# Optimization experiments

Hardware: AMD Instinct MI355X
Metric: run time of the kernel (lower is better)

The kernel has to match this reference:

```python
import jax, jax.numpy as jnp
import numpy as np

N, E, D, ED, H, DH = 30000, 480000, 128, 64, 8, 16  # nodes, edges, node dim, edge dim, heads, dim/head


def _bn(x, g, b):
    # BatchNorm1d training-mode math: biased batch stats over the node/edge axis
    m = jnp.mean(x, axis=0)
    v = jnp.mean(jnp.square(x - m), axis=0)
    return g * (x - m) * jax.lax.rsqrt(v + 1e-5) + b


def setup_inputs() -> dict:
    key = jax.random.key(0)
    ks = jax.random.split(key, 32)
    w = lambda k, shp: (jax.random.normal(k, shp, dtype=jnp.float32) * 0.05)
    inp = {
        "x": jax.random.normal(ks[0], (N, D), dtype=jnp.float32),
        "edge_index": jax.random.randint(ks[1], (2, E), 0, N, dtype=jnp.int32),
        "edge_attr": jax.random.normal(ks[2], (E, ED), dtype=jnp.float32),
        # attention projections (use_bias=False)
        "Wq": w(ks[3], (D, D)), "Wk": w(ks[4], (D, D)), "Wv": w(ks[5], (D, D)),
        "We": w(ks[6], (ED, D)),
        # output / edge projections
        "W_Oh": w(ks[7], (D, D)), "b_Oh": jnp.zeros((D,), jnp.float32),
        "W_ep": w(ks[8], (H, ED)), "b_ep": jnp.zeros((ED,), jnp.float32),
        "W_Oe": w(ks[9], (ED, ED)), "b_Oe": jnp.zeros((ED,), jnp.float32),
        # FFNs
        "W_h1": w(ks[10], (D, 2 * D)), "b_h1": jnp.zeros((2 * D,), jnp.float32),
        "W_h2": w(ks[11], (2 * D, D)), "b_h2": jnp.zeros((D,), jnp.float32),
        "W_e1": w(ks[12], (ED, 2 * ED)), "b_e1": jnp.zeros((2 * ED,), jnp.float32),
        "W_e2": w(ks[13], (2 * ED, ED)), "b_e2": jnp.zeros((ED,), jnp.float32),
        # batch-norm affine params
        "g1h": jnp.ones((D,), jnp.float32), "B1h": jnp.zeros((D,), jnp.float32),
        "g1e": jnp.ones((ED,), jnp.float32), "B1e": jnp.zeros((ED,), jnp.float32),
        "g2h": jnp.ones((D,), jnp.float32), "B2h": jnp.zeros((D,), jnp.float32),
        "g2e": jnp.ones((ED,), jnp.float32), "B2e": jnp.zeros((ED,), jnp.float32),
    }
    return inp


def reference(x, edge_index, edge_attr, Wq, Wk, Wv, We,
              W_Oh, b_Oh, W_ep, b_ep, W_Oe, b_Oe,
              W_h1, b_h1, W_h2, b_h2, W_e1, b_e1, W_e2, b_e2,
              g1h, B1h, g1e, B1e, g2h, B2h, g2e, B2e):
    n = x.shape[0]
    e_n = edge_attr.shape[0]
    src, dst = edge_index[0], edge_index[1]

    # MultiHeadAttentionLayer
    Q = (x @ Wq).reshape(n, H, DH)
    K = (x @ Wk).reshape(n, H, DH)
    V = (x @ Wv).reshape(n, H, DH)
    Pe = (edge_attr @ We).reshape(e_n, H, DH)

    inv_sqrt_d = 1.0 / np.sqrt(DH).astype(np.float32)
    score = jnp.sum(Q[dst] * K[src] * inv_sqrt_d * Pe, axis=-1)  # [E, H]
    e_out = score
    sc = jnp.exp(jnp.clip(score, -5.0, 5.0))
    z = jax.ops.segment_sum(sc, dst, num_segments=n)            # [N, H]
    alpha = sc / (z[dst] + 1e-6)                                # [E, H]
    msg = V[src] * alpha[..., None]                             # [E, H, DH]
    h_attn = jax.ops.segment_sum(msg, dst, num_segments=n).reshape(n, H * DH)

    # edge_project on raw scores, then O projections (dropout=0)
    e = e_out @ W_ep + b_ep
    h = h_attn @ W_Oh + b_Oh
    e = e @ W_Oe + b_Oe

    # residual 1 (in_dim == out_dim, edge dims equal -> identity residuals)
    h = x + h
    e = edge_attr + e

    h = _bn(h, g1h, B1h)
    e = _bn(e, g1e, B1e)

    # FFNs with residual + BN
    h2 = h
    h = jax.nn.relu(h @ W_h1 + b_h1) @ W_h2 + b_h2
    h = _bn(h2 + h, g2h, B2h)

    e2 = e
    e = jax.nn.relu(e @ W_e1 + b_e1) @ W_e2 + b_e2
    e = _bn(e2 + e, g2e, B2e)

    return (h, e)
```

## Files before the change

kernel.cpp:

```cpp
#include <hip/hip_runtime.h>
#include <hip/hip_bf16.h>

typedef __hip_bfloat16 bf16;

#define NN 30000
#define NE 480000
#define DD 128
#define ED 64
#define NH 8

#define ST_SUM_H1 0
#define ST_SQ_H1  128
#define ST_SUM_H2 256
#define ST_SQ_H2  384
#define ST_SUM_E1 512
#define ST_SQ_E1  576
#define ST_SUM_E2 640
#define ST_SQ_E2  704
#define W_FLAG    768

#define W_HATT  241024
#define W_SC    4081024

#define CSR_DEG   12000000
#define CSR_ROW   12030000
#define CSR_CUR   12060004
#define CSR_ADJ   12100000

__device__ __forceinline__ float ldf(const void* p, long i, bool bf) {
  if (bf) return __bfloat162float(((const bf16*)p)[i]);
  return ((const float*)p)[i];
}

__global__ __launch_bounds__(64) void k_detect(const void* __restrict__ x, int* __restrict__ flag)
{
  int lane = threadIdx.x;
  unsigned w = ((const unsigned*)x)[lane];
  unsigned low = w & 0xFFFFu;
  unsigned el = (low >> 7) & 0xFFu;
  bool hit = (el >= 0x70u && el <= 0x86u);
  unsigned long long m = __ballot(hit);
  if (lane == 0) *flag = (__popcll(m) >= 32) ? 1 : 0;
}

__global__ __launch_bounds__(256) void k_deg(const int* __restrict__ ei, int* __restrict__ deg)
{
  int i = blockIdx.x * 256 + threadIdx.x;
  if (i < NE) atomicAdd(&deg[ei[NE + i]], 1);
}

__global__ __launch_bounds__(1024) void k_scan(
    const int* __restrict__ deg, int* __restrict__ rowptr, int* __restrict__ cursor)
{
  __shared__ int buf[1024];
  __shared__ int carry;
  int tid = threadIdx.x;
  if (tid == 0) carry = 0;
  __syncthreads();
  for (int c = 0; c < 30; ++c) {
    int i = c * 1024 + tid;
    int v = (i < NN) ? deg[i] : 0;
    buf[tid] = v;
    __syncthreads();
    for (int off = 1; off < 1024; off <<= 1) {
      int t = (tid >= off) ? buf[tid - off] : 0;
      __syncthreads();
      buf[tid] += t;
      __syncthreads();
    }
    int excl = carry + buf[tid] - v;
    if (i < NN) { rowptr[i] = excl; cursor[i] = excl; }
    if (i == NN) rowptr[NN] = excl;
    __syncthreads();
    if (tid == 1023) carry += buf[1023];
    __syncthreads();
  }
}

__global__ __launch_bounds__(256) void k_fill(
    const int* __restrict__ ei, int* __restrict__ cursor, int* __restrict__ adj)
{
  int i = blockIdx.x * 256 + threadIdx.x;
  if (i < NE) {
    int p = atomicAdd(&cursor[ei[NE + i]], 1);
    adj[p] = i;
  }
}

__global__ __launch_bounds__(128) void k_qkv(
    const void* __restrict__ x, const void* __restrict__ Wq,
    const void* __restrict__ Wk, const void* __restrict__ Wv,
    float* __restrict__ Q, float* __restrict__ Kb, float* __restrict__ V,
    const int* __restrict__ flag)
{
  const bool isbf = (*flag != 0);
  __shared__ float xs[128][36];
  int tid = threadIdx.x;
  int row0 = blockIdx.x * 32;
  int nrows = min(32, NN - row0);
  for (int r = 0; r < 32; ++r)
    xs[tid][r] = (r < nrows) ? ldf(x, (long)(row0 + r) * DD + tid, isbf) : 0.f;
  __syncthreads();
  int c0 = (tid & 63) * 2;
  int rh = (tid >> 6) * 16;
  const void* Ws[3] = {Wq, Wk, Wv};
  float* Os[3] = {Q, Kb, V};
  for (int mm = 0; mm < 3; ++mm) {
    const void* W = Ws[mm];
    float u0[16], u1[16];
    #pragma unroll
    for (int r = 0; r < 16; ++r) { u0[r] = 0.f; u1[r] = 0.f; }
    #pragma unroll 4
    for (int k = 0; k < 128; ++k) {
      float w0 = ldf(W, (long)k * DD + c0, isbf);
      float w1 = ldf(W, (long)k * DD + c0 + 1, isbf);
      const float4* xp = (const float4*)&xs[k][rh];
      #pragma unroll
      for (int r4 = 0; r4 < 4; ++r4) {
        float4 x4 = xp[r4];
        u0[r4*4+0] += x4.x * w0; u1[r4*4+0] += x4.x * w1;
        u0[r4*4+1] += x4.y * w0; u1[r4*4+1] += x4.y * w1;
        u0[r4*4+2] += x4.z * w0; u1[r4*4+2] += x4.z * w1;
        u0[r4*4+3] += x4.w * w0; u1[r4*4+3] += x4.w * w1;
      }
    }
    float* O = Os[mm];
    #pragma unroll
    for (int r = 0; r < 16; ++r) {
      if (rh + r < nrows)
        *(float2*)&O[(long)(row0 + rh + r) * DD + c0] = make_float2(u0[r], u1[r]);
    }
  }
}

__global__ __launch_bounds__(128) void k_edge_score(
    const int* __restrict__ ei, const void* __restrict__ ea,
    const void* __restrict__ We, const float* __restrict__ Q,
    const float* __restrict__ Kb,
    float* __restrict__ score, const int* __restrict__ flag)
{
  const bool isbf = (*flag != 0);
  __shared__ float es[64][36];
  __shared__ int sd_s[32], sd_d[32];
  int tid = threadIdx.x;
  long e0 = (long)blockIdx.x * 32;
  #pragma unroll
  for (int i = 0; i < 16; ++i) {
    int idx = i * 128 + tid;
    es[idx & 63][idx >> 6] = ldf(ea, e0 * ED + idx, isbf);
  }
  if (tid < 32) sd_s[tid] = ei[e0 + tid];
  else if (tid < 64) sd_d[tid - 32] = ei[NE + e0 + (tid - 32)];
  __syncthreads();
  float pe[32];
  #pragma unroll
  for (int r = 0; r < 32; ++r) pe[r] = 0.f;
  #pragma unroll 4
  for (int k = 0; k < 64; ++k) {
    float w = ldf(We, (long)k * DD + tid, isbf);
    const float4* ep = (const float4*)&es[k][0];
    #pragma unroll
    for (int r4 = 0; r4 < 8; ++r4) {
      float4 e4 = ep[r4];
      pe[r4*4+0] += e4.x * w; pe[r4*4+1] += e4.y * w;
      pe[r4*4+2] += e4.z * w; pe[r4*4+3] += e4.w * w;
    }
  }
  int h = tid >> 4;
  bool lead = (tid & 15) == 0;
  #pragma unroll 4
  for (int r = 0; r < 32; ++r) {
    int s = sd_s[r], d = sd_d[r];
    float q  = Q [(long)d * DD + tid];
    float kk = Kb[(long)s * DD + tid];
    float sv = q * kk * pe[r];
    sv += __shfl_xor(sv, 1);
    sv += __shfl_xor(sv, 2);
    sv += __shfl_xor(sv, 4);
    sv += __shfl_xor(sv, 8);
    if (lead) score[(e0 + r) * NH + h] = sv * 0.25f;
  }
}

__global__ __launch_bounds__(256) void k_aggregate(
    const int* __restrict__ ei, const float* __restrict__ V,
    const float* __restrict__ score, const int* __restrict__ rowptr,
    const int* __restrict__ adj, float* __restrict__ hatt)
{
  int lane = threadIdx.x & 63;
  int wv = threadIdx.x >> 6;
  int d = blockIdx.x * 4 + wv;
  if (d >= NN) return;
  int p0 = rowptr[d], p1 = rowptr[d + 1];
  int hsh = lane >> 3;
  float a0 = 0.f, a1 = 0.f, zh = 0.f;
  for (int p = p0; p < p1; ++p) {
    int e = adj[p];
    int s = ei[e];
    float sc = score[(long)e * NH + hsh];
    float ec = __expf(fminf(fmaxf(sc, -5.f), 5.f));
    float2 v = *(const float2*)(V + (long)s * DD + 2 * lane);
    a0 += ec * v.x; a1 += ec * v.y; zh += ec;
  }
  float inv = 1.f / (zh + 1e-6f);
  *(float2*)(hatt + (long)d * DD + 2 * lane) = make_float2(a0 * inv, a1 * inv);
}

__global__ __launch_bounds__(128) void k_edge_proj(
    const void* __restrict__ ea, const float* __restrict__ score,
    const void* __restrict__ W_ep, const void* __restrict__ b_ep,
    const void* __restrict__ W_Oe, const void* __restrict__ b_Oe,
    float* __restrict__ eout, float* __restrict__ stats,
    const int* __restrict__ flag)
{
  const bool isbf = (*flag != 0);
  __shared__ float sc[32][9];
  __shared__ float ep_lds[64][36];
  __shared__ float rs[2][64], rq[2][64];
  int tid = threadIdx.x;
  int j = tid & 63, wv = tid >> 6, rh = wv * 16;
  float bep = ldf(b_ep, j, isbf), boe = ldf(b_Oe, j, isbf);
  float wep[8];
  #pragma unroll
  for (int hh = 0; hh < 8; ++hh) wep[hh] = ldf(W_ep, hh * ED + j, isbf);
  float lsum = 0.f, lsq = 0.f;
  for (int t = blockIdx.x; t < NE / 32; t += gridDim.x) {
    long e0 = (long)t * 32;
    __syncthreads();
    #pragma unroll
    for (int i = 0; i < 2; ++i) {
      int idx = i * 128 + tid;
      sc[idx >> 3][idx & 7] = score[e0 * NH + idx];
    }
    __syncthreads();
    float u[16];
    #pragma unroll
    for (int r = 0; r < 16; ++r) u[r] = bep;
    #pragma unroll
    for (int hh = 0; hh < 8; ++hh) {
      float w = wep[hh];
      #pragma unroll
      for (int r = 0; r < 16; ++r) u[r] += sc[rh + r][hh] * w;
    }
    #pragma unroll
    for (int r = 0; r < 16; ++r) ep_lds[j][rh + r] = u[r];
    __syncthreads();
    float acc[16];
    #pragma unroll
    for (int r = 0; r < 16; ++r) acc[r] = 0.f;
    #pragma unroll 4
    for (int k = 0; k < 64; ++k) {
      float w = ldf(W_Oe, (long)k * ED + j, isbf);
      const float4* up = (const float4*)&ep_lds[k][rh];
      #pragma unroll
      for (int r4 = 0; r4 < 4; ++r4) {
        float4 u4 = up[r4];
        acc[r4*4+0] += u4.x * w; acc[r4*4+1] += u4.y * w;
        acc[r4*4+2] += u4.z * w; acc[r4*4+3] += u4.w * w;
      }
    }
    #pragma unroll
    for (int r = 0; r < 16; ++r) {
      float v = ldf(ea, (e0 + rh + r) * ED + j, isbf) + acc[r] + boe;
      eout[(e0 + rh + r) * ED + j] = v;
      lsum += v; lsq += v * v;
    }
  }
  rs[wv][j] = lsum; rq[wv][j] = lsq;
  __syncthreads();
  if (wv == 0) {
    atomicAdd(&stats[ST_SUM_E1 + j], rs[0][j] + rs[1][j]);
    atomicAdd(&stats[ST_SQ_E1 + j], rq[0][j] + rq[1][j]);
  }
}

__global__ __launch_bounds__(128) void k_hproj(
    const float* __restrict__ hatt, const void* __restrict__ x,
    const void* __restrict__ W_Oh, const void* __restrict__ b_Oh,
    float* __restrict__ hout, float* __restrict__ stats,
    const int* __restrict__ flag)
{
  const bool isbf = (*flag != 0);
  __shared__ float hs[128][36];
  __shared__ float ssum[2][128], ssq[2][128];
  int tid = threadIdx.x;
  int row0 = blockIdx.x * 32;
  int nrows = min(32, NN - row0);
  for (int r = 0; r < 32; ++r)
    hs[tid][r] = (r < nrows) ? hatt[(long)(row0 + r) * DD + tid] : 0.f;
  __syncthreads();
  int c0 = (tid & 63) * 2;
  int wv = tid >> 6;
  int rh = wv * 16;
  float u0[16], u1[16];
  #pragma unroll
  for (int r = 0; r < 16; ++r) { u0[r] = 0.f; u1[r] = 0.f; }
  #pragma unroll 4
  for (int k = 0; k < 128; ++k) {
    float w0 = ldf(W_Oh, (long)k * DD + c0, isbf);
    float w1 = ldf(W_Oh, (long)k * DD + c0 + 1, isbf);
    const float4* hp = (const float4*)&hs[k][rh];
    #pragma unroll
    for (int r4 = 0; r4 < 4; ++r4) {
      float4 h4 = hp[r4];
      u0[r4*4+0] += h4.x * w0; u1[r4*4+0] += h4.x * w1;
      u0[r4*4+1] += h4.y * w0; u1[r4*4+1] += h4.y * w1;
      u0[r4*4+2] += h4.z * w0; u1[r4*4+2] += h4.z * w1;
      u0[r4*4+3] += h4.w * w0; u1[r4*4+3] += h4.w * w1;
    }
  }
  float bo0 = ldf(b_Oh, c0, isbf), bo1 = ldf(b_Oh, c0 + 1, isbf);
  float s0 = 0.f, q0 = 0.f, s1 = 0.f, q1 = 0.f;
  #pragma unroll
  for (int r = 0; r < 16; ++r) {
    if (rh + r < nrows) {
      long row = row0 + rh + r;
      float v0 = ldf(x, row * DD + c0, isbf) + u0[r] + bo0;
      float v1 = ldf(x, row * DD + c0 + 1, isbf) + u1[r] + bo1;
      *(float2*)&hout[row * DD + c0] = make_float2(v0, v1);
      s0 += v0; q0 += v0 * v0; s1 += v1; q1 += v1 * v1;
    }
  }
  ssum[wv][c0] = s0; ssum[wv][c0 + 1] = s1;
  ssq[wv][c0] = q0;  ssq[wv][c0 + 1] = q1;
  __syncthreads();
  atomicAdd(&stats[ST_SUM_H1 + tid], ssum[0][tid] + ssum[1][tid]);
  atomicAdd(&stats[ST_SQ_H1 + tid], ssq[0][tid] + ssq[1][tid]);
}

__global__ __launch_bounds__(128) void k_hffn(
    float* __restrict__ hio,
    const void* __restrict__ g1h, const void* __restrict__ B1h,
    const void* __restrict__ W_h1, const void* __restrict__ b_h1,
    const void* __restrict__ W_h2, const void* __restrict__ b_h2,
    float* __restrict__ stats, const int* __restrict__ flag)
{
  const bool isbf = (*flag != 0);
  __shared__ float hb[128][36];
  __shared__ float uu[256][36];
  __shared__ float ssum[2][128], ssq[2][128];
  int tid = threadIdx.x;
  int row0 = blockIdx.x * 32;
  int nrows = min(32, NN - row0);
  float m = stats[ST_SUM_H1 + tid] * (1.0f / NN);
  float var = stats[ST_SQ_H1 + tid] * (1.0f / NN) - m * m;
  float rstd = rsqrtf(fmaxf(var, 0.f) + 1e-5f);
  float g = ldf(g1h, tid, isbf), B = ldf(B1h, tid, isbf);
  for (int r = 0; r < 32; ++r) {
    float v = (r < nrows) ? hio[(long)(row0 + r) * DD + tid] : 0.f;
    hb[tid][r] = g * (v - m) * rstd + B;
  }
  __syncthreads();
  float u0[32], u1[32];
  #pragma unroll
  for (int r = 0; r < 32; ++r) { u0[r] = 0.f; u1[r] = 0.f; }
  #pragma unroll 2
  for (int k = 0; k < 128; ++k) {
    float w0 = ldf(W_h1, (long)k * 256 + tid, isbf);
    float w1 = ldf(W_h1, (long)k * 256 + 128 + tid, isbf);
    const float4* hp = (const float4*)&hb[k][0];
    #pragma unroll
    for (int r4 = 0; r4 < 8; ++r4) {
      float4 h4 = hp[r4];
      u0[r4*4+0] += h4.x * w0; u1[r4*4+0] += h4.x * w1;
      u0[r4*4+1] += h4.y * w0; u1[r4*4+1] += h4.y * w1;
      u0[r4*4+2] += h4.z * w0; u1[r4*4+2] += h4.z * w1;
      u0[r4*4+3] += h4.w * w0; u1[r4*4+3] += h4.w * w1;
    }
  }
  float bu0 = ldf(b_h1, tid, isbf), bu1 = ldf(b_h1, 128 + tid, isbf);
  for (int r = 0; r < 32; ++r) {
    uu[tid][r]       = fmaxf(u0[r] + bu0, 0.f);
    uu[128 + tid][r] = fmaxf(u1[r] + bu1, 0.f);
  }
  __syncthreads();
  int c0 = (tid & 63) * 2;
  int wv2 = tid >> 6;
  int rh2 = wv2 * 16;
  float f0[16], f1[16];
  #pragma unroll
  for (int r = 0; r < 16; ++r) { f0[r] = 0.f; f1[r] = 0.f; }
  #pragma unroll 2
  for (int jj = 0; jj < 256; ++jj) {
    float w0 = ldf(W_h2, (long)jj * DD + c0, isbf);
    float w1 = ldf(W_h2, (long)jj * DD + c0 + 1, isbf);
    const float4* up = (const float4*)&uu[jj][rh2];
    #pragma unroll
    for (int r4 = 0; r4 < 4; ++r4) {
      float4 u4 = up[r4];
      f0[r4*4+0] += u4.x * w0; f1[r4*4+0] += u4.x * w1;
      f0[r4*4+1] += u4.y * w0; f1[r4*4+1] += u4.y * w1;
      f0[r4*4+2] += u4.z * w0; f1[r4*4+2] += u4.z * w1;
      f0[r4*4+3] += u4.w * w0; f1[r4*4+3] += u4.w * w1;
    }
  }
  float bf0 = ldf(b_h2, c0, isbf), bf1 = ldf(b_h2, c0 + 1, isbf);
  float s0 = 0.f, q0 = 0.f, s1 = 0.f, q1 = 0.f;
  #pragma unroll
  for (int r = 0; r < 16; ++r) {
    if (rh2 + r < nrows) {
      float t0 = hb[c0][rh2 + r] + f0[r] + bf0;
      float t1 = hb[c0 + 1][rh2 + r] + f1[r] + bf1;
      *(float2*)&hio[(long)(row0 + rh2 + r) * DD + c0] = make_float2(t0, t1);
      s0 += t0; q0 += t0 * t0; s1 += t1; q1 += t1 * t1;
    }
  }
  ssum[wv2][c0] = s0; ssum[wv2][c0 + 1] = s1;
  ssq[wv2][c0] = q0;  ssq[wv2][c0 + 1] = q1;
  __syncthreads();
  atomicAdd(&stats[ST_SUM_H2 + tid], ssum[0][tid] + ssum[1][tid]);
  atomicAdd(&stats[ST_SQ_H2 + tid], ssq[0][tid] + ssq[1][tid]);
}

__global__ __launch_bounds__(256) void k_hfinal(
    float* __restrict__ io, const void* __restrict__ g,
    const void* __restrict__ B, const float* __restrict__ stats,
    const int* __restrict__ flag)
{
  const bool isbf = (*flag != 0);
  long idx = ((long)blockIdx.x * 256 + threadIdx.x) * 4;
  int c = (int)(idx & (DD - 1));
  float4 v = *(float4*)(io + idx);
  float o[4] = {v.x, v.y, v.z, v.w};
  #pragma unroll
  for (int j = 0; j < 4; ++j) {
    int cc = c + j;
    float m = stats[ST_SUM_H2 + cc] * (1.0f / NN);
    float var = stats[ST_SQ_H2 + cc] * (1.0f / NN) - m * m;
    float rstd = rsqrtf(fmaxf(var, 0.f) + 1e-5f);
    o[j] = ldf(g, cc, isbf) * (o[j] - m) * rstd + ldf(B, cc, isbf);
  }
  *(float4*)(io + idx) = make_float4(o[0], o[1], o[2], o[3]);
}

__global__ __launch_bounds__(128) void k_effn(
    float* __restrict__ eio,
    const void* __restrict__ g1e, const void* __restrict__ B1e,
    const void* __restrict__ W_e1, const void* __restrict__ b_e1,
    const void* __restrict__ W_e2, const void* __restrict__ b_e2,
    float* __restrict__ stats, const int* __restrict__ flag)
{
  const bool isbf = (*flag != 0);
  __shared__ float es[64][36];
  __shared__ float uu[128][36];
  __shared__ float rs[2][64], rq[2][64];
  int tid = threadIdx.x;
  int f = tid & 63;
  int wv = tid >> 6;
  int rh = wv * 16;
  long row0 = (long)blockIdx.x * 32;
  float m = stats[ST_SUM_E1 + f] * (1.0f / NE);
  float var = stats[ST_SQ_E1 + f] * (1.0f / NE) - m * m;
  float rstd = rsqrtf(fmaxf(var, 0.f) + 1e-5f);
  float g = ldf(g1e, f, isbf), B = ldf(B1e, f, isbf);
  #pragma unroll
  for (int r = 0; r < 16; ++r) {
    float v = eio[(row0 + rh + r) * ED + f];
    es[f][rh + r] = g * (v - m) * rstd + B;
  }
  __syncthreads();
  float u[32];
  #pragma unroll
  for (int r = 0; r < 32; ++r) u[r] = 0.f;
  #pragma unroll 4
  for (int k = 0; k < 64; ++k) {
    float w = ldf(W_e1, (long)k * 128 + tid, isbf);
    const float4* ep = (const float4*)&es[k][0];
    #pragma unroll
    for (int r4 = 0; r4 < 8; ++r4) {
      float4 e4 = ep[r4];
      u[r4*4+0] += e4.x * w; u[r4*4+1] += e4.y * w;
      u[r4*4+2] += e4.z * w; u[r4*4+3] += e4.w * w;
    }
  }
  float bu = ldf(b_e1, tid, isbf);
  #pragma unroll
  for (int r = 0; r < 32; ++r) uu[tid][r] = fmaxf(u[r] + bu, 0.f);
  __syncthreads();
  float acc[16];
  #pragma unroll
  for (int r = 0; r < 16; ++r) acc[r] = 0.f;
  #pragma unroll 4
  for (int j = 0; j < 128; ++j) {
    float w = ldf(W_e2, (long)j * ED + f, isbf);
    const float4* up = (const float4*)&uu[j][rh];
    #pragma unroll
    for (int r4 = 0; r4 < 4; ++r4) {
      float4 u4 = up[r4];
      acc[r4*4+0] += u4.x * w; acc[r4*4+1] += u4.y * w;
      acc[r4*4+2] += u4.z * w; acc[r4*4+3] += u4.w * w;
    }
  }
  float bf2 = ldf(b_e2, f, isbf);
  float lsum = 0.f, lsq = 0.f;
  #pragma unroll
  for (int r = 0; r < 16; ++r) {
    float t = es[f][rh + r] + acc[r] + bf2;
    eio[(row0 + rh + r) * ED + f] = t;
    lsum += t; lsq += t * t;
  }
  rs[wv][f] = lsum; rq[wv][f] = lsq;
  __syncthreads();
  if (wv == 0) {
    atomicAdd(&stats[ST_SUM_E2 + f], rs[0][f] + rs[1][f]);
    atomicAdd(&stats[ST_SQ_E2 + f], rq[0][f] + rq[1][f]);
  }
}

__global__ __launch_bounds__(256) void k_efinal(
    float* __restrict__ io, const void* __restrict__ g,
    const void* __restrict__ B, const float* __restrict__ stats,
    const int* __restrict__ flag)
{
  const bool isbf = (*flag != 0);
  long idx = ((long)blockIdx.x * 256 + threadIdx.x) * 4;
  int c = (int)(idx & (ED - 1));
  float4 v = *(float4*)(io + idx);
  float o[4] = {v.x, v.y, v.z, v.w};
  #pragma unroll
  for (int j = 0; j < 4; ++j) {
    int cc = c + j;
    float m = stats[ST_SUM_E2 + cc] * (1.0f / NE);
    float var = stats[ST_SQ_E2 + cc] * (1.0f / NE) - m * m;
    float rstd = rsqrtf(fmaxf(var, 0.f) + 1e-5f);
    o[j] = ldf(g, cc, isbf) * (o[j] - m) * rstd + ldf(B, cc, isbf);
  }
  *(float4*)(io + idx) = make_float4(o[0], o[1], o[2], o[3]);
}

extern "C" void kernel_launch(void* const* d_in, const int* in_sizes, int n_in,
                              void* d_out, int out_size, void* d_ws, size_t ws_size,
                              hipStream_t stream) {
  const void* x    = d_in[0];
  const int*  ei   = (const int*)d_in[1];
  const void* ea   = d_in[2];
  const void* Wq   = d_in[3];
  const void* Wk   = d_in[4];
  const void* Wv   = d_in[5];
  const void* We   = d_in[6];
  const void* W_Oh = d_in[7];
  const void* b_Oh = d_in[8];
  const void* W_ep = d_in[9];
  const void* b_ep = d_in[10];
  const void* W_Oe = d_in[11];
  const void* b_Oe = d_in[12];
  const void* W_h1 = d_in[13];
  const void* b_h1 = d_in[14];
  const void* W_h2 = d_in[15];
  const void* b_h2 = d_in[16];
  const void* W_e1 = d_in[17];
  const void* b_e1 = d_in[18];
  const void* W_e2 = d_in[19];
  const void* b_e2 = d_in[20];
  const void* g1h  = d_in[21];
  const void* B1h  = d_in[22];
  const void* g1e  = d_in[23];
  const void* B1e  = d_in[24];
  const void* g2h  = d_in[25];
  const void* B2h  = d_in[26];
  const void* g2e  = d_in[27];
  const void* B2e  = d_in[28];

  float* ws    = (float*)d_ws;
  float* stats = ws;
  int*   flag  = (int*)(ws + W_FLAG);
  float* hatt  = ws + W_HATT;
  float* score = ws + W_SC;

  float* out  = (float*)d_out;
  float* hout = out;
  float* eout = out + (size_t)NN * DD;
  float* Q    = out;
  float* Kb   = out + 3840000;
  float* V    = out + 7680000;
  int* deg    = (int*)out + CSR_DEG;
  int* rowptr = (int*)out + CSR_ROW;
  int* cursor = (int*)out + CSR_CUR;
  int* adj    = (int*)out + CSR_ADJ;

  hipMemsetAsync(ws, 0, 1024 * sizeof(float), stream);
  hipMemsetAsync(deg, 0, NN * sizeof(int), stream);
  k_detect<<<1, 64, 0, stream>>>(x, flag);

  k_deg <<<1875, 256, 0, stream>>>(ei, deg);
  k_scan<<<1, 1024, 0, stream>>>(deg, rowptr, cursor);
  k_fill<<<1875, 256, 0, stream>>>(ei, cursor, adj);

  k_qkv<<<938, 128, 0, stream>>>(x, Wq, Wk, Wv, Q, Kb, V, flag);
  k_edge_score<<<15000, 128, 0, stream>>>(ei, ea, We, Q, Kb, score, flag);
  k_aggregate<<<7500, 256, 0, stream>>>(ei, V, score, rowptr, adj, hatt);
  k_edge_proj<<<2048, 128, 0, stream>>>(ea, score, W_ep, b_ep, W_Oe, b_Oe, eout, stats, flag);
  k_hproj<<<938, 128, 0, stream>>>(hatt, x, W_Oh, b_Oh, hout, stats, flag);
  k_hffn<<<938, 128, 0, stream>>>(hout, g1h, B1h, W_h1, b_h1, W_h2, b_h2, stats, flag);
  k_hfinal<<<3750, 256, 0, stream>>>(hout, g2h, B2h, stats, flag);
  k_effn<<<15000, 128, 0, stream>>>(eout, g1e, B1e, W_e1, b_e1, W_e2, b_e2, stats, flag);
  k_efinal<<<30000, 256, 0, stream>>>(eout, g2e, B2e, stats, flag);
}
```

Measured before the change: 1.830 ms.

## Run edge FFN on bf16 MFMA with pre-transposed swizzled weights in LDS

The edge FFN (64->128->64 over 480k edges) moves from scalar fp32 FMAs to bf16 MFMA 16x16x32 instructions. Weights are transposed and converted to bf16 once by a new prep kernel, then staged per block in XOR-swizzled LDS along with the BN-normalised edge tile. The intent is to cut the compute-bound FMA cost of this large kernel. In exchange, the intermediate and the residual are rounded to bf16, which adds precision loss when the inputs are fp32.

```diff
diff --git a/kernel.cpp b/kernel.cpp
--- a/kernel.cpp
+++ b/kernel.cpp
@@ -2,6 +2,8 @@
 #include <hip/hip_bf16.h>
 
 typedef __hip_bfloat16 bf16;
+typedef __attribute__((ext_vector_type(8))) short short8v;
+typedef __attribute__((ext_vector_type(4))) float f32x4;
 
 #define NN 30000
 #define NE 480000
@@ -19,6 +21,8 @@
 #define ST_SQ_E2  704
 #define W_FLAG    768
 
+#define W_W1T   1024
+#define W_W2T   5120
 #define W_HATT  241024
 #define W_SC    4081024
 
@@ -30,6 +34,15 @@
 __device__ __forceinline__ float ldf(const void* p, long i, bool bf) {
   if (bf) return __bfloat162float(((const bf16*)p)[i]);
   return ((const float*)p)[i];
+}
+
+__device__ __forceinline__ unsigned short f2b(float f) {
+  unsigned u = __float_as_uint(f);
+  unsigned r = (u + 0x7FFFu + ((u >> 16) & 1u)) >> 16;
+  return (unsigned short)r;
+}
+__device__ __forceinline__ float b2f(unsigned short b) {
+  return __uint_as_float(((unsigned)b) << 16);
 }
 
 __global__ __launch_bounds__(64) void k_detect(const void* __restrict__ x, int* __restrict__ flag)
@@ -41,6 +54,23 @@
   bool hit = (el >= 0x70u && el <= 0x86u);
   unsigned long long m = __ballot(hit);
   if (lane == 0) *flag = (__popcll(m) >= 32) ? 1 : 0;
+}
+
+__global__ __launch_bounds__(256) void k_wprep(
+    const void* __restrict__ W_e1, const void* __restrict__ W_e2,
+    unsigned short* __restrict__ w1t, unsigned short* __restrict__ w2t,
+    const int* __restrict__ flag)
+{
+  const bool isbf = (*flag != 0);
+  int i = blockIdx.x * 256 + threadIdx.x;
+  if (i < 8192) {
+    int k = i >> 7, n = i & 127;
+    w1t[n * 64 + k] = f2b(ldf(W_e1, i, isbf));
+  } else {
+    int j = i - 8192;
+    int k = j >> 6, n = j & 63;
+    w2t[n * 128 + k] = f2b(ldf(W_e2, j, isbf));
+  }
 }
 
 __global__ __launch_bounds__(256) void k_deg(const int* __restrict__ ei, int* __restrict__ deg)
@@ -433,77 +463,134 @@
   *(float4*)(io + idx) = make_float4(o[0], o[1], o[2], o[3]);
 }
 
-__global__ __launch_bounds__(128) void k_effn(
+__global__ __launch_bounds__(256) void k_effn(
     float* __restrict__ eio,
     const void* __restrict__ g1e, const void* __restrict__ B1e,
-    const void* __restrict__ W_e1, const void* __restrict__ b_e1,
-    const void* __restrict__ W_e2, const void* __restrict__ b_e2,
+    const unsigned short* __restrict__ w1t, const unsigned short* __restrict__ w2t,
+    const void* __restrict__ b_e1, const void* __restrict__ b_e2,
     float* __restrict__ stats, const int* __restrict__ flag)
 {
   const bool isbf = (*flag != 0);
-  __shared__ float es[64][36];
-  __shared__ float uu[128][36];
-  __shared__ float rs[2][64], rq[2][64];
+  __shared__ unsigned short es[64 * 64];
+  __shared__ unsigned short uu[64 * 128];
+  __shared__ unsigned short w1[128 * 64];
+  __shared__ unsigned short w2[64 * 128];
+  __shared__ float ssum[4][64], ssq[4][64];
   int tid = threadIdx.x;
-  int f = tid & 63;
-  int wv = tid >> 6;
-  int rh = wv * 16;
-  long row0 = (long)blockIdx.x * 32;
-  float m = stats[ST_SUM_E1 + f] * (1.0f / NE);
-  float var = stats[ST_SQ_E1 + f] * (1.0f / NE) - m * m;
-  float rstd = rsqrtf(fmaxf(var, 0.f) + 1e-5f);
-  float g = ldf(g1e, f, isbf), B = ldf(B1e, f, isbf);
-  #pragma unroll
-  for (int r = 0; r < 16; ++r) {
-    float v = eio[(row0 + rh + r) * ED + f];
-    es[f][rh + r] = g * (v - m) * rstd + B;
-  }
-  __syncthreads();
-  float u[32];
-  #pragma unroll
-  for (int r = 0; r < 32; ++r) u[r] = 0.f;
-  #pragma unroll 4
-  for (int k = 0; k < 64; ++k) {
-    float w = ldf(W_e1, (long)k * 128 + tid, isbf);
-    const float4* ep = (const float4*)&es[k][0];
-    #pragma unroll
-    for (int r4 = 0; r4 < 8; ++r4) {
-      float4 e4 = ep[r4];
-      u[r4*4+0] += e4.x * w; u[r4*4+1] += e4.y * w;
-      u[r4*4+2] += e4.z * w; u[r4*4+3] += e4.w * w;
-    }
-  }
-  float bu = ldf(b_e1, tid, isbf);
-  #pragma unroll
-  for (int r = 0; r < 32; ++r) uu[tid][r] = fmaxf(u[r] + bu, 0.f);
-  __syncthreads();
-  float acc[16];
-  #pragma unroll
-  for (int r = 0; r < 16; ++r) acc[r] = 0.f;
-  #pragma unroll 4
-  for (int j = 0; j < 128; ++j) {
-    float w = ldf(W_e2, (long)j * ED + f, isbf);
-    const float4* up = (const float4*)&uu[j][rh];
-    #pragma unroll
-    for (int r4 = 0; r4 < 4; ++r4) {
-      float4 u4 = up[r4];
-      acc[r4*4+0] += u4.x * w; acc[r4*4+1] += u4.y * w;
-      acc[r4*4+2] += u4.z * w; acc[r4*4+3] += u4.w * w;
-    }
-  }
-  float bf2 = ldf(b_e2, f, isbf);
-  float lsum = 0.f, lsq = 0.f;
-  #pragma unroll
-  for (int r = 0; r < 16; ++r) {
-    float t = es[f][rh + r] + acc[r] + bf2;
-    eio[(row0 + rh + r) * ED + f] = t;
-    lsum += t; lsq += t * t;
-  }
-  rs[wv][f] = lsum; rq[wv][f] = lsq;
-  __syncthreads();
-  if (wv == 0) {
-    atomicAdd(&stats[ST_SUM_E2 + f], rs[0][f] + rs[1][f]);
-    atomicAdd(&stats[ST_SQ_E2 + f], rq[0][f] + rq[1][f]);
+  int lane = tid & 63, w = tid >> 6;
+  int ml = lane & 15, kg = lane >> 4;
+  long e0 = (long)blockIdx.x * 64;
+  {
+    unsigned* du = (unsigned*)w1;
+    int k2 = (tid & 31) * 2;
+    #pragma unroll
+    for (int it = 0; it < 16; ++it) {
+      int widx = it * 256 + tid;
+      int n = widx >> 5;
+      unsigned v = ((const unsigned*)w1t)[widx];
+      du[(n * 64 + (k2 ^ ((n & 7) << 3))) >> 1] = v;
+    }
+  }
+  {
+    unsigned* du = (unsigned*)w2;
+    int k2 = (tid & 63) * 2;
+    #pragma unroll
+    for (int it = 0; it < 16; ++it) {
+      int widx = it * 256 + tid;
+      int n = widx >> 6;
+      unsigned v = ((const unsigned*)w2t)[widx];
+      du[(n * 128 + (k2 ^ ((n & 7) << 3))) >> 1] = v;
+    }
+  }
+  {
+    unsigned* du = (unsigned*)es;
+    int c2 = (tid & 31) * 2;
+    float m0 = stats[ST_SUM_E1 + c2] * (1.0f / NE);
+    float v0 = stats[ST_SQ_E1 + c2] * (1.0f / NE) - m0 * m0;
+    float r0 = rsqrtf(fmaxf(v0, 0.f) + 1e-5f);
+    float g0 = ldf(g1e, c2, isbf), B0 = ldf(B1e, c2, isbf);
+    float m1 = stats[ST_SUM_E1 + c2 + 1] * (1.0f / NE);
+    float v1 = stats[ST_SQ_E1 + c2 + 1] * (1.0f / NE) - m1 * m1;
+    float r1 = rsqrtf(fmaxf(v1, 0.f) + 1e-5f);
+    float g1 = ldf(g1e, c2 + 1, isbf), B1 = ldf(B1e, c2 + 1, isbf);
+    #pragma unroll
+    for (int it = 0; it < 8; ++it) {
+      int widx = it * 256 + tid;
+      int r = widx >> 5;
+      float2 v = *(const float2*)(eio + (e0 + r) * 64 + c2);
+      unsigned short b0 = f2b(g0 * (v.x - m0) * r0 + B0);
+      unsigned short b1 = f2b(g1 * (v.y - m1) * r1 + B1);
+      du[(r * 64 + (c2 ^ ((r & 7) << 3))) >> 1] = (unsigned)b0 | ((unsigned)b1 << 16);
+    }
+  }
+  __syncthreads();
+  short8v a1[2];
+  #pragma unroll
+  for (int kt = 0; kt < 2; ++kt) {
+    int row = w * 16 + ml;
+    a1[kt] = *(short8v*)&es[row * 64 + ((kt * 32 + kg * 8) ^ ((row & 7) << 3))];
+  }
+  f32x4 acc1[8];
+  #pragma unroll
+  for (int nt = 0; nt < 8; ++nt) acc1[nt] = (f32x4){0.f, 0.f, 0.f, 0.f};
+  #pragma unroll
+  for (int nt = 0; nt < 8; ++nt) {
+    #pragma unroll
+    for (int kt = 0; kt < 2; ++kt) {
+      int n = nt * 16 + ml;
+      short8v b = *(short8v*)&w1[n * 64 + ((kt * 32 + kg * 8) ^ ((n & 7) << 3))];
+      acc1[nt] = __builtin_amdgcn_mfma_f32_16x16x32_bf16(a1[kt], b, acc1[nt], 0, 0, 0);
+    }
+  }
+  #pragma unroll
+  for (int nt = 0; nt < 8; ++nt) {
+    float bb = ldf(b_e1, nt * 16 + ml, isbf);
+    #pragma unroll
+    for (int rg = 0; rg < 4; ++rg) {
+      int row = w * 16 + kg * 4 + rg;
+      int col = nt * 16 + ml;
+      uu[row * 128 + (col ^ ((row & 7) << 3))] = f2b(fmaxf(acc1[nt][rg] + bb, 0.f));
+    }
+  }
+  short8v a2[4];
+  #pragma unroll
+  for (int kt = 0; kt < 4; ++kt) {
+    int row = w * 16 + ml;
+    a2[kt] = *(short8v*)&uu[row * 128 + ((kt * 32 + kg * 8) ^ ((row & 7) << 3))];
+  }
+  f32x4 acc2[4];
+  #pragma unroll
+  for (int nt = 0; nt < 4; ++nt) acc2[nt] = (f32x4){0.f, 0.f, 0.f, 0.f};
+  #pragma unroll
+  for (int nt = 0; nt < 4; ++nt) {
+    #pragma unroll
+    for (int kt = 0; kt < 4; ++kt) {
+      int n = nt * 16 + ml;
+      short8v b = *(short8v*)&w2[n * 128 + ((kt * 32 + kg * 8) ^ ((n & 7) << 3))];
+      acc2[nt] = __builtin_amdgcn_mfma_f32_16x16x32_bf16(a2[kt], b, acc2[nt], 0, 0, 0);
+    }
+  }
+  #pragma unroll
+  for (int nt = 0; nt < 4; ++nt) {
+    int col = nt * 16 + ml;
+    float bb = ldf(b_e2, col, isbf);
+    float s = 0.f, q = 0.f;
+    #pragma unroll
+    for (int rg = 0; rg < 4; ++rg) {
+      int row = w * 16 + kg * 4 + rg;
+      float resv = b2f(es[row * 64 + (col ^ ((row & 7) << 3))]);
+      float t = resv + acc2[nt][rg] + bb;
+      eio[(e0 + row) * 64 + col] = t;
+      s += t; q += t * t;
+    }
+    s += __shfl_xor(s, 16); s += __shfl_xor(s, 32);
+    q += __shfl_xor(q, 16); q += __shfl_xor(q, 32);
+    if (kg == 0) { ssum[w][col] = s; ssq[w][col] = q; }
+  }
+  __syncthreads();
+  if (tid < 64) {
+    atomicAdd(&stats[ST_SUM_E2 + tid], ssum[0][tid] + ssum[1][tid] + ssum[2][tid] + ssum[3][tid]);
+    atomicAdd(&stats[ST_SQ_E2 + tid],  ssq[0][tid] + ssq[1][tid] + ssq[2][tid] + ssq[3][tid]);
   }
 }
 
@@ -564,6 +651,8 @@
   float* ws    = (float*)d_ws;
   float* stats = ws;
   int*   flag  = (int*)(ws + W_FLAG);
+  unsigned short* w1t = (unsigned short*)(ws + W_W1T);
+  unsigned short* w2t = (unsigned short*)(ws + W_W2T);
   float* hatt  = ws + W_HATT;
   float* score = ws + W_SC;
 
@@ -581,6 +670,7 @@
   hipMemsetAsync(ws, 0, 1024 * sizeof(float), stream);
   hipMemsetAsync(deg, 0, NN * sizeof(int), stream);
   k_detect<<<1, 64, 0, stream>>>(x, flag);
+  k_wprep<<<64, 256, 0, stream>>>(W_e1, W_e2, w1t, w2t, flag);
 
   k_deg <<<1875, 256, 0, stream>>>(ei, deg);
   k_scan<<<1, 1024, 0, stream>>>(deg, rowptr, cursor);
@@ -593,6 +683,6 @@
   k_hproj<<<938, 128, 0, stream>>>(hatt, x, W_Oh, b_Oh, hout, stats, flag);
   k_hffn<<<938, 128, 0, stream>>>(hout, g1h, B1h, W_h1, b_h1, W_h2, b_h2, stats, flag);
   k_hfinal<<<3750, 256, 0, stream>>>(hout, g2h, B2h, stats, flag);
-  k_effn<<<15000, 128, 0, stream>>>(eout, g1e, B1e, W_e1, b_e1, W_e2, b_e2, stats, flag);
+  k_effn<<<7500, 256, 0, stream>>>(eout, g1e, B1e, w1t, w2t, b_e1, b_e2, stats, flag);
   k_efinal<<<30000, 256, 0, stream>>>(eout, g2e, B2e, stats, flag);
 }
```

Result: faster. 1.606 ms (-12.3%).
